# Optimization experiments

Measured on AMD Instinct MI355X. Metric: run time of the kernel, lower is better.

Reference implementation:

```python
import jax, jax.numpy as jnp
import numpy as np
from jax import lax

LATENT = 64
NUM_EMB = 512
BETA = 0.25
DN = ('NCHW', 'OIHW', 'NCHW')


def conv(x, w, b, stride, pad):
    y = lax.conv_general_dilated(x, w, (stride, stride), [(pad, pad), (pad, pad)],
                                 dimension_numbers=DN)
    return y + b[None, :, None, None]


def tconv(x, w, b, stride, pad, opad):
    # torch ConvTranspose2d(k=3, stride, padding=pad, output_padding=opad)
    # == dilated conv with lhs_dilation=stride, padding (k-1-pad, k-1-pad+opad),
    #    spatially-flipped kernel. w is stored OIHW (out, in, kh, kw).
    k = w.shape[2]
    lo, hi = k - 1 - pad, k - 1 - pad + opad
    y = lax.conv_general_dilated(x, w[:, :, ::-1, ::-1], (1, 1), [(lo, hi), (lo, hi)],
                                 lhs_dilation=(stride, stride), dimension_numbers=DN)
    return y + b[None, :, None, None]


def vector_quantize(z, codebook):
    # z: (B, D, H, W); codebook: (K, D)
    B, D, H, W = z.shape
    flat = z.transpose(0, 2, 3, 1).reshape(-1, D)  # (BHW, D)
    d = (jnp.sum(flat ** 2, axis=1, keepdims=True)
         + jnp.sum(codebook ** 2, axis=1)
         - 2.0 * flat @ codebook.T)  # (BHW, K)
    idx = jnp.argmin(d, axis=1)
    q = codebook[idx].reshape(B, H, W, D).transpose(0, 3, 1, 2)  # (B, D, H, W)
    commitment = jnp.mean((lax.stop_gradient(q) - z) ** 2)
    codebook_loss = jnp.mean((q - lax.stop_gradient(z)) ** 2)
    loss = BETA * commitment + codebook_loss
    q_ste = z + lax.stop_gradient(q - z)  # straight-through estimator
    return q_ste, loss


def setup_inputs() -> dict:
    key = jax.random.key(0)
    ks = jax.random.split(key, 16)
    f32 = jnp.float32
    inp = {
        'x': jax.random.uniform(ks[0], (1024, 1, 50, 50), dtype=f32),
        'enc_w1': jax.random.normal(ks[1], (32, 1, 3, 3), f32) * 0.1,
        'enc_b1': jnp.zeros((32,), f32),
        'enc_w2': jax.random.normal(ks[2], (64, 32, 3, 3), f32) * 0.05,
        'enc_b2': jnp.zeros((64,), f32),
        'enc_w3': jax.random.normal(ks[3], (LATENT, 64, 1, 1), f32) * 0.1,
        'enc_b3': jnp.zeros((LATENT,), f32),
        'codebook': jax.random.uniform(ks[4], (NUM_EMB, LATENT), dtype=f32),
        'dec_w1': jax.random.normal(ks[5], (64, LATENT, 3, 3), f32) * 0.05,
        'dec_b1': jnp.zeros((64,), f32),
        'dec_w2': jax.random.normal(ks[6], (32, 64, 3, 3), f32) * 0.05,
        'dec_b2': jnp.zeros((32,), f32),
        'dec_w3': jax.random.normal(ks[7], (1, 32, 3, 3), f32) * 0.05,
        'dec_b3': jnp.zeros((1,), f32),
    }
    return inp


def reference(x, enc_w1, enc_b1, enc_w2, enc_b2, enc_w3, enc_b3, codebook,
              dec_w1, dec_b1, dec_w2, dec_b2, dec_w3, dec_b3):
    # encoder: (B,1,50,50) -> (B,LATENT,13,13)
    h = jax.nn.relu(conv(x, enc_w1, enc_b1, 2, 1))
    h = jax.nn.relu(conv(h, enc_w2, enc_b2, 2, 1))
    z = conv(h, enc_w3, enc_b3, 1, 0)
    q, vq_loss = vector_quantize(z, codebook)
    # decoder: 13 -> 25 -> 50
    h = jax.nn.relu(tconv(q, dec_w1, dec_b1, 2, 1, 0))
    h = jax.nn.relu(tconv(h, dec_w2, dec_b2, 2, 1, 1))
    x_recon = jax.nn.sigmoid(conv(h, dec_w3, dec_b3, 1, 1))
    return x_recon, vq_loss
```

## Files before the change

### kernel.cpp

```cpp
#include <hip/hip_runtime.h>
#include <math.h>


typedef __attribute__((ext_vector_type(8))) short s8v;
typedef __attribute__((ext_vector_type(4))) float f4v;
typedef __attribute__((ext_vector_type(4))) int i4v;

__device__ inline unsigned short f2bf(float f) {
    unsigned u = __builtin_bit_cast(unsigned, f);
    return (unsigned short)((u + 0x7fffu + ((u >> 16) & 1u)) >> 16);
}
__device__ inline float bf2f(unsigned short h) {
    return __builtin_bit_cast(float, ((unsigned)h) << 16);
}

__global__ __launch_bounds__(256) void k_prep_all(
        const float* __restrict__ cb,  const float* __restrict__ ew2,
        const float* __restrict__ ew3, const float* __restrict__ dw1,
        const float* __restrict__ dw2,
        unsigned short* __restrict__ cbm, unsigned short* __restrict__ wB2n,
        unsigned short* __restrict__ wB1, unsigned short* __restrict__ wB2,
        unsigned short* __restrict__ wB3, float* __restrict__ cn,
        float* __restrict__ loss) {
    int i = blockIdx.x * 256 + threadIdx.x;
    if (i < 98304) {
        int j = i & 7, lane = (i >> 3) & 63;
        int kc = (i >> 9) % 6, nt = (i >> 9) / 6;
        int n = nt * 16 + (lane & 15);
        int k = kc * 32 + ((lane >> 4) << 3) + j;
        int seg = k >> 6, kk = k & 63;
        float c = cb[n * 64 + kk];
        unsigned short ch = f2bf(c);
        cbm[i] = (seg == 1) ? f2bf(c - bf2f(ch)) : ch;
    } else if (i < 153600) {
        int q = i - 98304;
        int j = q & 7, lane = (q >> 3) & 63;
        int kc = (q >> 9) % 27, nt = (q >> 9) / 27;
        int k = kc * 32 + ((lane >> 4) << 3) + j;
        int co = nt * 16 + (lane & 15);
        int part = (k < 288) ? 0 : (k < 576) ? 1 : 0;
        int kk = (k < 288) ? k : (k < 576) ? k - 288 : k - 576;
        int tap = kk >> 5, ci = kk & 31;
        float v = ew2[(co * 32 + ci) * 9 + tap];
        unsigned short hi = f2bf(v);
        wB2n[q] = part ? f2bf(v - bf2f(hi)) : hi;
    } else if (i < 219136) {
        int q = i - 153600;
        int j = q & 7, l = (q >> 3) & 63, kc = (q >> 9) & 7, nt = q >> 12;
        int n = nt * 16 + (l & 15), k = kc * 32 + (l >> 4) * 8 + j;
        int cls = n >> 6, co = n & 63, p = k >> 6, ci = k & 63;
        int jh = -1, jw = -1;
        if (cls == 0)      { if (p == 0) { jh = 1; jw = 1; } }
        else if (cls == 1) { if (p == 1) { jh = 1; jw = 0; } else if (p == 0) { jh = 1; jw = 2; } }
        else if (cls == 2) { if (p == 2) { jh = 0; jw = 1; } else if (p == 0) { jh = 2; jw = 1; } }
        else { if (p == 3) { jh = 0; jw = 0; } else if (p == 2) { jh = 0; jw = 2; }
               else if (p == 1) { jh = 2; jw = 0; } else { jh = 2; jw = 2; } }
        float v = (jh >= 0) ? dw1[((co * 64 + ci) * 3 + jh) * 3 + jw] : 0.f;
        wB1[q] = f2bf(v);
    } else if (i < 251904) {
        int q = i - 219136;
        int j = q & 7, l = (q >> 3) & 63, kc = (q >> 9) & 7, nt = q >> 12;
        int n = nt * 16 + (l & 15), k = kc * 32 + (l >> 4) * 8 + j;
        int cls = n >> 5, co = n & 31, p = k >> 6, ci = k & 63;
        int jh = -1, jw = -1;
        if (cls == 0)      { if (p == 0) { jh = 1; jw = 1; } }
        else if (cls == 1) { if (p == 1) { jh = 1; jw = 0; } else if (p == 0) { jh = 1; jw = 2; } }
        else if (cls == 2) { if (p == 2) { jh = 0; jw = 1; } else if (p == 0) { jh = 2; jw = 1; } }
        else { if (p == 3) { jh = 0; jw = 0; } else if (p == 2) { jh = 0; jw = 2; }
               else if (p == 1) { jh = 2; jw = 0; } else { jh = 2; jw = 2; } }
        float v = (jh >= 0) ? dw2[((co * 64 + ci) * 3 + jh) * 3 + jw] : 0.f;
        wB2[q] = f2bf(v);
    } else if (i < 264192) {
        int q = i - 251904;
        int j = q & 7, lane = (q >> 3) & 63;
        int kc = (q >> 9) % 6, nt = (q >> 9) / 6;
        int k = kc * 32 + ((lane >> 4) << 3) + j;
        int n = nt * 16 + (lane & 15);
        int part = (k < 64) ? 0 : (k < 128) ? 1 : 0;
        int kk = (k < 64) ? k : (k < 128) ? k - 64 : k - 128;
        float v = ew3[n * 64 + kk];
        unsigned short hi = f2bf(v);
        wB3[q] = part ? f2bf(v - bf2f(hi)) : hi;
    } else if (i < 264704) {
        int k = i - 264192;
        const float* r = cb + k * 64;
        float s = 0.f;
#pragma unroll
        for (int c = 0; c < 64; ++c) s += r[c] * r[c];
        cn[k] = s;
    } else if (i == 264704) {
        *loss = 0.f;
    }
}

__global__ __launch_bounds__(256) void k_conv1(const float* __restrict__ x,
                                               const float* __restrict__ w,
                                               const float* __restrict__ b,
                                               float* __restrict__ h1, int total) {
    __shared__ float4 wl4[72];
    float* wl = (float*)wl4;
    int tid = threadIdx.x;
    for (int t = tid; t < 288; t += 256) {
        int tap = t >> 5, co = t & 31;
        wl[t] = w[co * 9 + tap];
    }
    __syncthreads();
    int pix = blockIdx.x * 256 + tid;
    if (pix >= total) return;
    int n = pix / 625, p = pix % 625, oh = p / 25, ow = p % 25;
    const float* xp = x + (size_t)n * 2500;
    float4 a[8];
#pragma unroll
    for (int j = 0; j < 8; ++j) a[j] = ((const float4*)b)[j];
#pragma unroll
    for (int kh = 0; kh < 3; ++kh) {
        int ih = 2 * oh - 1 + kh;
        if ((unsigned)ih >= 50u) continue;
#pragma unroll
        for (int kw = 0; kw < 3; ++kw) {
            int iw = 2 * ow - 1 + kw;
            if ((unsigned)iw >= 50u) continue;
            float v = xp[ih * 50 + iw];
            int tap = kh * 3 + kw;
#pragma unroll
            for (int j = 0; j < 8; ++j) {
                float4 ww = wl4[tap * 8 + j];
                a[j].x += v * ww.x; a[j].y += v * ww.y;
                a[j].z += v * ww.z; a[j].w += v * ww.w;
            }
        }
    }
    float4* op = (float4*)(h1 + (size_t)pix * 32);
#pragma unroll
    for (int j = 0; j < 8; ++j) {
        float4 r;
        r.x = fmaxf(a[j].x, 0.f); r.y = fmaxf(a[j].y, 0.f);
        r.z = fmaxf(a[j].z, 0.f); r.w = fmaxf(a[j].w, 0.f);
        op[j] = r;
    }
}

__global__ __launch_bounds__(256) void k_enc_m(const float* __restrict__ h1,
                                               const unsigned short* __restrict__ B2n,
                                               const unsigned short* __restrict__ B3,
                                               const float* __restrict__ b2,
                                               const float* __restrict__ b3,
                                               float* __restrict__ z, int npix) {
    __shared__ short a1[16 * 872];
    __shared__ short a2[16 * 200];
    __shared__ float cz[16 * 68];
    int tid = threadIdx.x, blk = blockIdx.x;
    {
        int m = tid >> 4, chunk = tid & 15;
        if (chunk < 9) {
            int pix = blk * 16 + m;
            float4 v[8];
            const float4 zero = {0.f, 0.f, 0.f, 0.f};
            bool ok = false;
            if (pix < npix) {
                int n = pix / 169, p = pix % 169, oh = p / 13, ow = p % 13;
                int kh = chunk / 3, kw = chunk % 3;
                int ih = 2 * oh - 1 + kh, iw = 2 * ow - 1 + kw;
                ok = ((unsigned)ih < 25u) && ((unsigned)iw < 25u);
                if (ok) {
                    const float4* ip = (const float4*)(h1 + (((size_t)n * 25 + ih) * 25 + iw) * 32);
#pragma unroll
                    for (int c4 = 0; c4 < 8; ++c4) v[c4] = ip[c4];
                }
            }
            if (!ok) {
#pragma unroll
                for (int c4 = 0; c4 < 8; ++c4) v[c4] = zero;
            }
            unsigned short hi[32], lo[32];
#pragma unroll
            for (int c4 = 0; c4 < 8; ++c4) {
                float vv[4] = {v[c4].x, v[c4].y, v[c4].z, v[c4].w};
#pragma unroll
                for (int e = 0; e < 4; ++e) {
                    int ci = c4 * 4 + e;
                    unsigned short h = f2bf(vv[e]);
                    hi[ci] = h;
                    lo[ci] = f2bf(vv[e] - bf2f(h));
                }
            }
            short* row = a1 + m * 872 + chunk * 32;
            i4v* d0 = (i4v*)row;
            i4v* d1 = (i4v*)(row + 288);
            i4v* d2 = (i4v*)(row + 576);
#pragma unroll
            for (int g = 0; g < 4; ++g) {
                i4v ph, pl;
#pragma unroll
                for (int e = 0; e < 4; ++e) {
                    int b0 = g * 8 + e * 2;
                    ph[e] = (int)((unsigned)hi[b0] | ((unsigned)hi[b0 + 1] << 16));
                    pl[e] = (int)((unsigned)lo[b0] | ((unsigned)lo[b0 + 1] << 16));
                }
                d0[g] = ph; d1[g] = ph; d2[g] = pl;
            }
        }
    }
    __syncthreads();
    int wave = tid >> 6, lane = tid & 63;
    int arow1 = (lane & 15) * 872 + (lane >> 4) * 8;
    f4v acc = (f4v){0.f, 0.f, 0.f, 0.f};
#pragma unroll
    for (int kc = 0; kc < 27; ++kc) {
        s8v a = *(const s8v*)(a1 + arow1 + kc * 32);
        s8v b = *(const s8v*)((const short*)B2n + ((size_t)((wave * 27 + kc) * 64 + lane)) * 8);
        acc = __builtin_amdgcn_mfma_f32_16x16x32_bf16(a, b, acc, 0, 0, 0);
    }
    {
        float bv = b2[wave * 16 + (lane & 15)];
        int n = wave * 16 + (lane & 15);
#pragma unroll
        for (int r = 0; r < 4; ++r) {
            int m = (lane >> 4) * 4 + r;
            float h = fmaxf(acc[r] + bv, 0.f);
            unsigned short hh = f2bf(h);
            unsigned short ll = f2bf(h - bf2f(hh));
            a2[m * 200 + n] = (short)hh;
            a2[m * 200 + 64 + n] = (short)hh;
            a2[m * 200 + 128 + n] = (short)ll;
        }
    }
    __syncthreads();
    int arow2 = (lane & 15) * 200 + (lane >> 4) * 8;
    f4v acc2 = (f4v){0.f, 0.f, 0.f, 0.f};
#pragma unroll
    for (int kc = 0; kc < 6; ++kc) {
        s8v a = *(const s8v*)(a2 + arow2 + kc * 32);
        s8v b = *(const s8v*)((const short*)B3 + ((size_t)((wave * 6 + kc) * 64 + lane)) * 8);
        acc2 = __builtin_amdgcn_mfma_f32_16x16x32_bf16(a, b, acc2, 0, 0, 0);
    }
    {
        float bv = b3[wave * 16 + (lane & 15)];
        int n = wave * 16 + (lane & 15);
#pragma unroll
        for (int r = 0; r < 4; ++r) {
            int m = (lane >> 4) * 4 + r;
            cz[m * 68 + n] = acc2[r] + bv;
        }
    }
    __syncthreads();
    {
        int m = tid >> 4, c4 = tid & 15;
        int pix = blk * 16 + m;
        if (pix < npix) {
            float4 v = *(float4*)(cz + m * 68 + c4 * 4);
            *(float4*)(z + (size_t)pix * 64 + c4 * 4) = v;
        }
    }
}

__global__ __launch_bounds__(256) void k_vq_m(const float* __restrict__ z,
                                              const float* __restrict__ cb,
                                              const unsigned short* __restrict__ cbm,
                                              const float* __restrict__ cn,
                                              float* __restrict__ q,
                                              float* __restrict__ loss, int npix) {
    __shared__ short a_lds[32 * 200];
    __shared__ float reds[4 * 32];
    __shared__ int   redk[4 * 32];
    __shared__ int   bkf[32];
    __shared__ float lred[4];
    int tid = threadIdx.x, blk = blockIdx.x;
    {
        int m = tid >> 3, p = tid & 7;
        int pix = blk * 32 + m;
        unsigned short zh[8], zl[8];
        if (pix < npix) {
            const float* src = z + (size_t)pix * 64 + p * 8;
#pragma unroll
            for (int v = 0; v < 8; ++v) {
                float f = src[v];
                unsigned short h = f2bf(f);
                zh[v] = h; zl[v] = f2bf(f - bf2f(h));
            }
        } else {
#pragma unroll
            for (int v = 0; v < 8; ++v) { zh[v] = 0; zl[v] = 0; }
        }
        unsigned ph[4], pl[4];
#pragma unroll
        for (int v = 0; v < 4; ++v) {
            ph[v] = (unsigned)zh[2 * v] | ((unsigned)zh[2 * v + 1] << 16);
            pl[v] = (unsigned)zl[2 * v] | ((unsigned)zl[2 * v + 1] << 16);
        }
        short* row = a_lds + m * 200;
        i4v vh = (i4v){(int)ph[0], (int)ph[1], (int)ph[2], (int)ph[3]};
        i4v vl = (i4v){(int)pl[0], (int)pl[1], (int)pl[2], (int)pl[3]};
        *(i4v*)(row + p * 8) = vh;
        *(i4v*)(row + 64 + p * 8) = vh;
        *(i4v*)(row + 128 + p * 8) = vl;
    }
    __syncthreads();
    int wave = tid >> 6, lane = tid & 63;
    s8v af[2][6];
#pragma unroll
    for (int mt = 0; mt < 2; ++mt) {
        int arow = (mt * 16 + (lane & 15)) * 200 + (lane >> 4) * 8;
#pragma unroll
        for (int kc = 0; kc < 6; ++kc)
            af[mt][kc] = *(const s8v*)(a_lds + arow + kc * 32);
    }
    float bd[2][4];
    int bk[2][4];
#pragma unroll
    for (int mt = 0; mt < 2; ++mt)
#pragma unroll
        for (int r = 0; r < 4; ++r) { bd[mt][r] = 3.4e38f; bk[mt][r] = 0; }
#pragma unroll 2
    for (int nt = 0; nt < 8; ++nt) {
        int ntg = wave * 8 + nt;
        s8v bf[6];
#pragma unroll
        for (int kc = 0; kc < 6; ++kc)
            bf[kc] = *(const s8v*)((const short*)cbm + ((size_t)((ntg * 6 + kc) * 64 + lane)) * 8);
        f4v acc0 = (f4v){0.f, 0.f, 0.f, 0.f};
        f4v acc1 = (f4v){0.f, 0.f, 0.f, 0.f};
#pragma unroll
        for (int kc = 0; kc < 6; ++kc) {
            acc0 = __builtin_amdgcn_mfma_f32_16x16x32_bf16(af[0][kc], bf[kc], acc0, 0, 0, 0);
            acc1 = __builtin_amdgcn_mfma_f32_16x16x32_bf16(af[1][kc], bf[kc], acc1, 0, 0, 0);
        }
        int kcol = ntg * 16 + (lane & 15);
        float cnk = cn[kcol];
#pragma unroll
        for (int r = 0; r < 4; ++r) {
            float d0 = cnk - 2.f * acc0[r];
            if (d0 < bd[0][r]) { bd[0][r] = d0; bk[0][r] = kcol; }
            float d1 = cnk - 2.f * acc1[r];
            if (d1 < bd[1][r]) { bd[1][r] = d1; bk[1][r] = kcol; }
        }
    }
#pragma unroll
    for (int off = 1; off < 16; off <<= 1) {
#pragma unroll
        for (int mt = 0; mt < 2; ++mt)
#pragma unroll
            for (int r = 0; r < 4; ++r) {
                float od = __shfl_xor(bd[mt][r], off);
                int ok = __shfl_xor(bk[mt][r], off);
                if (od < bd[mt][r] || (od == bd[mt][r] && ok < bk[mt][r])) {
                    bd[mt][r] = od; bk[mt][r] = ok;
                }
            }
    }
    if ((lane & 15) == 0) {
#pragma unroll
        for (int mt = 0; mt < 2; ++mt)
#pragma unroll
            for (int r = 0; r < 4; ++r) {
                int m = mt * 16 + (lane >> 4) * 4 + r;
                reds[wave * 32 + m] = bd[mt][r];
                redk[wave * 32 + m] = bk[mt][r];
            }
    }
    __syncthreads();
    if (tid < 32) {
        float d0 = reds[tid]; int k0 = redk[tid];
#pragma unroll
        for (int w = 1; w < 4; ++w) {
            float dw = reds[w * 32 + tid]; int kw = redk[w * 32 + tid];
            if (dw < d0 || (dw == d0 && kw < k0)) { d0 = dw; k0 = kw; }
        }
        bkf[tid] = k0;
    }
    __syncthreads();
    float lsum = 0.f;
#pragma unroll
    for (int it = 0; it < 2; ++it) {
        int m = tid >> 3, c4 = (tid & 7) + it * 8;
        int pix = blk * 32 + m;
        if (pix < npix) {
            int k0 = bkf[m];
            float4 cq = ((const float4*)cb)[(size_t)k0 * 16 + c4];
            float4 zz = ((const float4*)(z + (size_t)pix * 64))[c4];
            float dx = cq.x - zz.x, dy = cq.y - zz.y, dz = cq.z - zz.z, dw = cq.w - zz.w;
            lsum += dx * dx + dy * dy + dz * dz + dw * dw;
            ((float4*)(q + (size_t)pix * 64))[c4] = cq;
        }
    }
#pragma unroll
    for (int off = 32; off > 0; off >>= 1) lsum += __shfl_down(lsum, off);
    if ((tid & 63) == 0) lred[tid >> 6] = lsum;
    __syncthreads();
    if (tid == 0) {
        float t = lred[0] + lred[1] + lred[2] + lred[3];
        atomicAdd(loss, t * (1.25f / 11075584.f));
    }
}

__global__ __launch_bounds__(256) void k_tconv1_m(const float* __restrict__ q,
                                                  const unsigned short* __restrict__ wB,
                                                  const float* __restrict__ bias,
                                                  unsigned short* __restrict__ d1,
                                                  int nquad) {
    __shared__ short a_lds[32 * 264];
    __shared__ short c_lds[32 * 264];
    int tid = threadIdx.x, blk = blockIdx.x;
#pragma unroll
    for (int pass = 0; pass < 4; ++pass) {
        int idx = tid + pass * 256;
        int m = idx >> 5, sub = idx & 31;
        int qg = blk * 32 + m;
        int p = sub >> 3, ci0 = (sub & 7) * 8;
        unsigned short t8[8];
        bool have = false;
        if (qg < nquad) {
            int img = qg / 169, r = qg % 169, qm = r / 13, qw = r % 13;
            int sm = qm + (p >> 1), sw = qw + (p & 1);
            if (sm < 13 && sw < 13) {
                const float* src = q + (((size_t)img * 13 + sm) * 13 + sw) * 64 + ci0;
#pragma unroll
                for (int v = 0; v < 8; ++v) t8[v] = f2bf(src[v]);
                have = true;
            }
        }
        if (!have) {
#pragma unroll
            for (int v = 0; v < 8; ++v) t8[v] = 0;
        }
        i4v pk;
#pragma unroll
        for (int e = 0; e < 4; ++e)
            pk[e] = (int)((unsigned)t8[2 * e] | ((unsigned)t8[2 * e + 1] << 16));
        *(i4v*)(a_lds + m * 264 + sub * 8) = pk;
    }
    __syncthreads();
    int wave = tid >> 6, lane = tid & 63;
    f4v acc[2][4];
#pragma unroll
    for (int mt = 0; mt < 2; ++mt)
#pragma unroll
        for (int i = 0; i < 4; ++i) acc[mt][i] = (f4v){0.f, 0.f, 0.f, 0.f};
    float bv[4];
#pragma unroll
    for (int i = 0; i < 4; ++i) bv[i] = bias[((wave * 4 + i) * 16 + (lane & 15)) & 63];
#pragma unroll
    for (int kc = 0; kc < 8; ++kc) {
        s8v a0 = *(const s8v*)(a_lds + ((lane & 15)) * 264 + (lane >> 4) * 8 + kc * 32);
        s8v a1 = *(const s8v*)(a_lds + (16 + (lane & 15)) * 264 + (lane >> 4) * 8 + kc * 32);
#pragma unroll
        for (int i = 0; i < 4; ++i) {
            int nt = wave * 4 + i;
            s8v b = *(const s8v*)((const short*)wB + ((size_t)((nt * 8 + kc) * 64 + lane)) * 8);
            acc[0][i] = __builtin_amdgcn_mfma_f32_16x16x32_bf16(a0, b, acc[0][i], 0, 0, 0);
            acc[1][i] = __builtin_amdgcn_mfma_f32_16x16x32_bf16(a1, b, acc[1][i], 0, 0, 0);
        }
    }
#pragma unroll
    for (int mt = 0; mt < 2; ++mt)
#pragma unroll
        for (int i = 0; i < 4; ++i) {
            int n = (wave * 4 + i) * 16 + (lane & 15);
#pragma unroll
            for (int r2 = 0; r2 < 4; ++r2) {
                int m = mt * 16 + (lane >> 4) * 4 + r2;
                float v = fmaxf(acc[mt][i][r2] + bv[i], 0.f);
                c_lds[m * 264 + n] = (short)f2bf(v);
            }
        }
    __syncthreads();
#pragma unroll
    for (int pass = 0; pass < 4; ++pass) {
        int ch = tid + pass * 256;
        int m = ch >> 5, cpart = ch & 31;
        int qg = blk * 32 + m;
        if (qg >= nquad) continue;
        int img = qg / 169, r = qg % 169, qm = r / 13, qw = r % 13;
        int cls = cpart >> 3, co8 = (cpart & 7) * 8;
        int oh = 2 * qm + (cls >> 1), ow = 2 * qw + (cls & 1);
        if (oh >= 25 || ow >= 25) continue;
        i4v val = *(i4v*)(c_lds + m * 264 + cls * 64 + co8);
        *(i4v*)(d1 + (((size_t)img * 25 + oh) * 25 + ow) * 64 + co8) = val;
    }
}

__global__ __launch_bounds__(256) void k_tconv2_m(const unsigned short* __restrict__ d1,
                                                  const unsigned short* __restrict__ wB,
                                                  const float* __restrict__ bias,
                                                  unsigned short* __restrict__ d2,
                                                  int nquad) {
    __shared__ short a_lds[32 * 264];
    __shared__ short c_lds[32 * 136];
    int tid = threadIdx.x, blk = blockIdx.x;
#pragma unroll
    for (int pass = 0; pass < 4; ++pass) {
        int idx = tid + pass * 256;
        int m = idx >> 5, sub = idx & 31;
        int qg = blk * 32 + m;
        int p = sub >> 3, ci0 = (sub & 7) * 8;
        i4v v = (i4v){0, 0, 0, 0};
        if (qg < nquad) {
            int img = qg / 625, r = qg % 625, qm = r / 25, qw = r % 25;
            int sm = qm + (p >> 1), sw = qw + (p & 1);
            if (sm < 25 && sw < 25)
                v = *(const i4v*)(d1 + (((size_t)img * 25 + sm) * 25 + sw) * 64 + ci0);
        }
        *(i4v*)(a_lds + m * 264 + sub * 8) = v;
    }
    __syncthreads();
    int wave = tid >> 6, lane = tid & 63;
    f4v acc[2][2];
#pragma unroll
    for (int mt = 0; mt < 2; ++mt)
#pragma unroll
        for (int i = 0; i < 2; ++i) acc[mt][i] = (f4v){0.f, 0.f, 0.f, 0.f};
    float bv[2];
#pragma unroll
    for (int i = 0; i < 2; ++i) bv[i] = bias[((wave * 2 + i) * 16 + (lane & 15)) & 31];
#pragma unroll
    for (int kc = 0; kc < 8; ++kc) {
        s8v a0 = *(const s8v*)(a_lds + ((lane & 15)) * 264 + (lane >> 4) * 8 + kc * 32);
        s8v a1 = *(const s8v*)(a_lds + (16 + (lane & 15)) * 264 + (lane >> 4) * 8 + kc * 32);
#pragma unroll
        for (int i = 0; i < 2; ++i) {
            int nt = wave * 2 + i;
            s8v b = *(const s8v*)((const short*)wB + ((size_t)((nt * 8 + kc) * 64 + lane)) * 8);
            acc[0][i] = __builtin_amdgcn_mfma_f32_16x16x32_bf16(a0, b, acc[0][i], 0, 0, 0);
            acc[1][i] = __builtin_amdgcn_mfma_f32_16x16x32_bf16(a1, b, acc[1][i], 0, 0, 0);
        }
    }
#pragma unroll
    for (int mt = 0; mt < 2; ++mt)
#pragma unroll
        for (int i = 0; i < 2; ++i) {
            int n = (wave * 2 + i) * 16 + (lane & 15);
#pragma unroll
            for (int r2 = 0; r2 < 4; ++r2) {
                int m = mt * 16 + (lane >> 4) * 4 + r2;
                float v = fmaxf(acc[mt][i][r2] + bv[i], 0.f);
                c_lds[m * 136 + n] = (short)f2bf(v);
            }
        }
    __syncthreads();
#pragma unroll
    for (int pass = 0; pass < 2; ++pass) {
        int ch = tid + pass * 256;
        int m = ch >> 4, cpart = ch & 15;
        int qg = blk * 32 + m;
        if (qg >= nquad) continue;
        int img = qg / 625, r = qg % 625, qm = r / 25, qw = r % 25;
        int cls = cpart >> 2, co8 = (cpart & 3) * 8;
        int oh = 2 * qm + (cls >> 1), ow = 2 * qw + (cls & 1);
        i4v val = *(i4v*)(c_lds + m * 136 + cls * 32 + co8);
        *(i4v*)(d2 + (((size_t)img * 50 + oh) * 50 + ow) * 32 + co8) = val;
    }
}

__global__ __launch_bounds__(256) void k_convf(const unsigned short* __restrict__ in,
                                               const float* __restrict__ w,
                                               const float* __restrict__ b,
                                               float* __restrict__ out, int total) {
    __shared__ float wl[288];
    int tid = threadIdx.x;
    for (int t = tid; t < 288; t += 256) {
        int tap = t >> 5, ci = t & 31;
        wl[t] = w[ci * 9 + tap];
    }
    __syncthreads();
    int pix = blockIdx.x * 256 + tid;
    if (pix >= total) return;
    int n = pix / 2500, p = pix % 2500, oh = p / 50, ow = p % 50;
    float acc = b[0];
#pragma unroll
    for (int kh = 0; kh < 3; ++kh) {
        int ih = oh - 1 + kh;
        if ((unsigned)ih >= 50u) continue;
#pragma unroll
        for (int kw = 0; kw < 3; ++kw) {
            int iw = ow - 1 + kw;
            if ((unsigned)iw >= 50u) continue;
            const float* wt = wl + (kh * 3 + kw) * 32;
            const i4v* ip4 = (const i4v*)(in + (((size_t)n * 50 + ih) * 50 + iw) * 32);
#pragma unroll
            for (int c8 = 0; c8 < 4; ++c8) {
                i4v u = ip4[c8];
#pragma unroll
                for (int e = 0; e < 4; ++e) {
                    unsigned uu = (unsigned)u[e];
                    float x0 = __builtin_bit_cast(float, uu << 16);
                    float x1 = __builtin_bit_cast(float, uu & 0xffff0000u);
                    acc = fmaf(x0, wt[c8 * 8 + e * 2], acc);
                    acc = fmaf(x1, wt[c8 * 8 + e * 2 + 1], acc);
                }
            }
        }
    }
    out[pix] = 1.f / (1.f + expf(-acc));
}

extern "C" void kernel_launch(void* const* d_in, const int* in_sizes, int n_in,
                              void* d_out, int out_size, void* d_ws, size_t ws_size,
                              hipStream_t stream) {
    const float* x   = (const float*)d_in[0];
    const float* ew1 = (const float*)d_in[1];
    const float* eb1 = (const float*)d_in[2];
    const float* ew2 = (const float*)d_in[3];
    const float* eb2 = (const float*)d_in[4];
    const float* ew3 = (const float*)d_in[5];
    const float* eb3 = (const float*)d_in[6];
    const float* cb  = (const float*)d_in[7];
    const float* dw1 = (const float*)d_in[8];
    const float* db1 = (const float*)d_in[9];
    const float* dw2 = (const float*)d_in[10];
    const float* db2 = (const float*)d_in[11];
    const float* dw3 = (const float*)d_in[12];
    const float* db3 = (const float*)d_in[13];
    float* out = (float*)d_out;
    float* loss = out + 2560000;

    float* ws = (float*)d_ws;
    float* cn = ws;
    unsigned short* wB1  = (unsigned short*)(ws + 512);
    unsigned short* wB2  = (unsigned short*)(ws + 33280);
    unsigned short* wB2n = (unsigned short*)(ws + 49664);
    unsigned short* wB3  = (unsigned short*)(ws + 77312);
    unsigned short* cbm  = (unsigned short*)(ws + 83456);
    const size_t tw_floats = 132608;

    const int B = 1024;
    const size_t A_per = 40000, B_per = 20000;
    size_t avail = (ws_size / 4 > tw_floats) ? ws_size / 4 - tw_floats : 0;
    int BC = (int)(avail / (A_per + B_per));
    if (BC > B) BC = B;
    if (BC < 1) BC = 1;
    float* regA = ws + tw_floats;
    float* regB = regA + (size_t)BC * A_per;

    k_prep_all<<<1035, 256, 0, stream>>>(cb, ew2, ew3, dw1, dw2,
                                         cbm, wB2n, wB1, wB2, wB3, cn, loss);

    for (int n0 = 0; n0 < B; n0 += BC) {
        int bc = (B - n0 < BC) ? (B - n0) : BC;
        const float* xch = x + (size_t)n0 * 2500;

        int t1 = bc * 625;
        k_conv1<<<(t1 + 255) / 256, 256, 0, stream>>>(xch, ew1, eb1, regA, t1);

        int npix = bc * 169;
        k_enc_m<<<(npix + 15) / 16, 256, 0, stream>>>(regA, wB2n, wB3, eb2, eb3, regB, npix);

        k_vq_m<<<(npix + 31) / 32, 256, 0, stream>>>(regB, cb, cbm, cn, regA, loss, npix);

        unsigned short* d1 = (unsigned short*)regB;
        k_tconv1_m<<<(npix + 31) / 32, 256, 0, stream>>>(regA, wB1, db1, d1, npix);

        int nq2 = bc * 625;
        unsigned short* d2 = (unsigned short*)regA;
        k_tconv2_m<<<(nq2 + 31) / 32, 256, 0, stream>>>(d1, wB2, db2, d2, nq2);

        int t6 = bc * 2500;
        k_convf<<<(t6 + 255) / 256, 256, 0, stream>>>(d2, dw3, db3, out + (size_t)n0 * 2500, t6);
    }
}
```

Before: 505.0 us.

## Store intermediates as pre-split bf16 hi/lo pairs instead of fp32

The conv1 output and the encoder latent are now written as bf16 hi/lo split pairs rather than fp32. Consumers can then copy them straight into LDS without re-splitting, and the split is no longer repeated for every 3x3 tap read in k_enc_m. The quantized output q is stored as single bf16, halving its traffic, and the VQ loss reconstructs z from the hi/lo copy already in LDS. Byte counts stay the same for h1 and z, so the gain comes mainly from removed conversion ALU work and the smaller q.

Measured after the change: 495.5 us. About the same (-1.9%).

```diff
diff --git a/kernel.cpp b/kernel.cpp
--- a/kernel.cpp
+++ b/kernel.cpp
@@ -5,6 +5,7 @@
 typedef __attribute__((ext_vector_type(8))) short s8v;
 typedef __attribute__((ext_vector_type(4))) float f4v;
 typedef __attribute__((ext_vector_type(4))) int i4v;
+typedef __attribute__((ext_vector_type(4))) short s4v;
 
 __device__ inline unsigned short f2bf(float f) {
     unsigned u = __builtin_bit_cast(unsigned, f);
@@ -96,7 +97,8 @@
 __global__ __launch_bounds__(256) void k_conv1(const float* __restrict__ x,
                                                const float* __restrict__ w,
                                                const float* __restrict__ b,
-                                               float* __restrict__ h1, int total) {
+                                               unsigned short* __restrict__ h1,
+                                               int total) {
     __shared__ float4 wl4[72];
     float* wl = (float*)wl4;
     int tid = threadIdx.x;
@@ -130,58 +132,61 @@
             }
         }
     }
-    float4* op = (float4*)(h1 + (size_t)pix * 32);
+    unsigned short hi[32], lo[32];
 #pragma unroll
     for (int j = 0; j < 8; ++j) {
-        float4 r;
-        r.x = fmaxf(a[j].x, 0.f); r.y = fmaxf(a[j].y, 0.f);
-        r.z = fmaxf(a[j].z, 0.f); r.w = fmaxf(a[j].w, 0.f);
-        op[j] = r;
-    }
-}
-
-__global__ __launch_bounds__(256) void k_enc_m(const float* __restrict__ h1,
+        float vv[4] = {a[j].x, a[j].y, a[j].z, a[j].w};
+#pragma unroll
+        for (int e = 0; e < 4; ++e) {
+            float v = fmaxf(vv[e], 0.f);
+            unsigned short h = f2bf(v);
+            hi[j * 4 + e] = h;
+            lo[j * 4 + e] = f2bf(v - bf2f(h));
+        }
+    }
+    i4v* op = (i4v*)(h1 + (size_t)pix * 64);
+#pragma unroll
+    for (int g = 0; g < 4; ++g) {
+        i4v ph, pl;
+#pragma unroll
+        for (int e = 0; e < 4; ++e) {
+            int b0 = g * 8 + e * 2;
+            ph[e] = (int)((unsigned)hi[b0] | ((unsigned)hi[b0 + 1] << 16));
+            pl[e] = (int)((unsigned)lo[b0] | ((unsigned)lo[b0 + 1] << 16));
+        }
+        op[g] = ph;
+        op[4 + g] = pl;
+    }
+}
+
+__global__ __launch_bounds__(256) void k_enc_m(const unsigned short* __restrict__ h1,
                                                const unsigned short* __restrict__ B2n,
                                                const unsigned short* __restrict__ B3,
                                                const float* __restrict__ b2,
                                                const float* __restrict__ b3,
-                                               float* __restrict__ z, int npix) {
+                                               unsigned short* __restrict__ z, int npix) {
     __shared__ short a1[16 * 872];
     __shared__ short a2[16 * 200];
-    __shared__ float cz[16 * 68];
+    __shared__ short czs[16 * 136];
     int tid = threadIdx.x, blk = blockIdx.x;
     {
         int m = tid >> 4, chunk = tid & 15;
         if (chunk < 9) {
             int pix = blk * 16 + m;
-            float4 v[8];
-            const float4 zero = {0.f, 0.f, 0.f, 0.f};
-            bool ok = false;
+            i4v vh[4], vl[4];
+#pragma unroll
+            for (int g = 0; g < 4; ++g) {
+                vh[g] = (i4v){0, 0, 0, 0};
+                vl[g] = (i4v){0, 0, 0, 0};
+            }
             if (pix < npix) {
                 int n = pix / 169, p = pix % 169, oh = p / 13, ow = p % 13;
                 int kh = chunk / 3, kw = chunk % 3;
                 int ih = 2 * oh - 1 + kh, iw = 2 * ow - 1 + kw;
-                ok = ((unsigned)ih < 25u) && ((unsigned)iw < 25u);
-                if (ok) {
-                    const float4* ip = (const float4*)(h1 + (((size_t)n * 25 + ih) * 25 + iw) * 32);
-#pragma unroll
-                    for (int c4 = 0; c4 < 8; ++c4) v[c4] = ip[c4];
-                }
-            }
-            if (!ok) {
-#pragma unroll
-                for (int c4 = 0; c4 < 8; ++c4) v[c4] = zero;
-            }
-            unsigned short hi[32], lo[32];
-#pragma unroll
-            for (int c4 = 0; c4 < 8; ++c4) {
-                float vv[4] = {v[c4].x, v[c4].y, v[c4].z, v[c4].w};
-#pragma unroll
-                for (int e = 0; e < 4; ++e) {
-                    int ci = c4 * 4 + e;
-                    unsigned short h = f2bf(vv[e]);
-                    hi[ci] = h;
-                    lo[ci] = f2bf(vv[e] - bf2f(h));
+                if (((unsigned)ih < 25u) && ((unsigned)iw < 25u)) {
+                    const i4v* ip = (const i4v*)(h1 + (((size_t)n * 25 + ih) * 25 + iw) * 64);
+#pragma unroll
+                    for (int g = 0; g < 4; ++g) { vh[g] = ip[g]; vl[g] = ip[4 + g]; }
                 }
             }
             short* row = a1 + m * 872 + chunk * 32;
@@ -189,16 +194,7 @@
             i4v* d1 = (i4v*)(row + 288);
             i4v* d2 = (i4v*)(row + 576);
 #pragma unroll
-            for (int g = 0; g < 4; ++g) {
-                i4v ph, pl;
-#pragma unroll
-                for (int e = 0; e < 4; ++e) {
-                    int b0 = g * 8 + e * 2;
-                    ph[e] = (int)((unsigned)hi[b0] | ((unsigned)hi[b0 + 1] << 16));
-                    pl[e] = (int)((unsigned)lo[b0] | ((unsigned)lo[b0 + 1] << 16));
-                }
-                d0[g] = ph; d1[g] = ph; d2[g] = pl;
-            }
+            for (int g = 0; g < 4; ++g) { d0[g] = vh[g]; d1[g] = vh[g]; d2[g] = vl[g]; }
         }
     }
     __syncthreads();
@@ -240,25 +236,26 @@
 #pragma unroll
         for (int r = 0; r < 4; ++r) {
             int m = (lane >> 4) * 4 + r;
-            cz[m * 68 + n] = acc2[r] + bv;
+            float v = acc2[r] + bv;
+            unsigned short hh = f2bf(v);
+            czs[m * 136 + n] = (short)hh;
+            czs[m * 136 + 64 + n] = (short)f2bf(v - bf2f(hh));
         }
     }
     __syncthreads();
     {
-        int m = tid >> 4, c4 = tid & 15;
+        int m = tid >> 4, t = tid & 15;
         int pix = blk * 16 + m;
-        if (pix < npix) {
-            float4 v = *(float4*)(cz + m * 68 + c4 * 4);
-            *(float4*)(z + (size_t)pix * 64 + c4 * 4) = v;
-        }
-    }
-}
-
-__global__ __launch_bounds__(256) void k_vq_m(const float* __restrict__ z,
+        if (pix < npix)
+            *(i4v*)(z + (size_t)pix * 128 + t * 8) = *(i4v*)(czs + m * 136 + t * 8);
+    }
+}
+
+__global__ __launch_bounds__(256) void k_vq_m(const unsigned short* __restrict__ z,
                                               const float* __restrict__ cb,
                                               const unsigned short* __restrict__ cbm,
                                               const float* __restrict__ cn,
-                                              float* __restrict__ q,
+                                              unsigned short* __restrict__ q,
                                               float* __restrict__ loss, int npix) {
     __shared__ short a_lds[32 * 200];
     __shared__ float reds[4 * 32];
@@ -269,28 +266,14 @@
     {
         int m = tid >> 3, p = tid & 7;
         int pix = blk * 32 + m;
-        unsigned short zh[8], zl[8];
+        i4v vh = (i4v){0, 0, 0, 0};
+        i4v vl = (i4v){0, 0, 0, 0};
         if (pix < npix) {
-            const float* src = z + (size_t)pix * 64 + p * 8;
-#pragma unroll
-            for (int v = 0; v < 8; ++v) {
-                float f = src[v];
-                unsigned short h = f2bf(f);
-                zh[v] = h; zl[v] = f2bf(f - bf2f(h));
-            }
-        } else {
-#pragma unroll
-            for (int v = 0; v < 8; ++v) { zh[v] = 0; zl[v] = 0; }
-        }
-        unsigned ph[4], pl[4];
-#pragma unroll
-        for (int v = 0; v < 4; ++v) {
-            ph[v] = (unsigned)zh[2 * v] | ((unsigned)zh[2 * v + 1] << 16);
-            pl[v] = (unsigned)zl[2 * v] | ((unsigned)zl[2 * v + 1] << 16);
+            const i4v* src = (const i4v*)(z + (size_t)pix * 128);
+            vh = src[p];
+            vl = src[8 + p];
         }
         short* row = a_lds + m * 200;
-        i4v vh = (i4v){(int)ph[0], (int)ph[1], (int)ph[2], (int)ph[3]};
-        i4v vl = (i4v){(int)pl[0], (int)pl[1], (int)pl[2], (int)pl[3]};
         *(i4v*)(row + p * 8) = vh;
         *(i4v*)(row + 64 + p * 8) = vh;
         *(i4v*)(row + 128 + p * 8) = vl;
@@ -377,10 +360,19 @@
         if (pix < npix) {
             int k0 = bkf[m];
             float4 cq = ((const float4*)cb)[(size_t)k0 * 16 + c4];
-            float4 zz = ((const float4*)(z + (size_t)pix * 64))[c4];
-            float dx = cq.x - zz.x, dy = cq.y - zz.y, dz = cq.z - zz.z, dw = cq.w - zz.w;
+            const short* rz = a_lds + m * 200 + c4 * 4;
+            s4v zh4 = *(const s4v*)rz;
+            s4v zl4 = *(const s4v*)(rz + 128);
+            float zx = bf2f((unsigned short)zh4[0]) + bf2f((unsigned short)zl4[0]);
+            float zy = bf2f((unsigned short)zh4[1]) + bf2f((unsigned short)zl4[1]);
+            float zz = bf2f((unsigned short)zh4[2]) + bf2f((unsigned short)zl4[2]);
+            float zw = bf2f((unsigned short)zh4[3]) + bf2f((unsigned short)zl4[3]);
+            float dx = cq.x - zx, dy = cq.y - zy, dz = cq.z - zz, dw = cq.w - zw;
             lsum += dx * dx + dy * dy + dz * dz + dw * dw;
-            ((float4*)(q + (size_t)pix * 64))[c4] = cq;
+            s4v qs;
+            qs[0] = (short)f2bf(cq.x); qs[1] = (short)f2bf(cq.y);
+            qs[2] = (short)f2bf(cq.z); qs[3] = (short)f2bf(cq.w);
+            *(s4v*)(q + (size_t)pix * 64 + c4 * 4) = qs;
         }
     }
 #pragma unroll
@@ -393,7 +385,7 @@
     }
 }
 
-__global__ __launch_bounds__(256) void k_tconv1_m(const float* __restrict__ q,
+__global__ __launch_bounds__(256) void k_tconv1_m(const unsigned short* __restrict__ q,
                                                   const unsigned short* __restrict__ wB,
                                                   const float* __restrict__ bias,
                                                   unsigned short* __restrict__ d1,
@@ -407,27 +399,14 @@
         int m = idx >> 5, sub = idx & 31;
         int qg = blk * 32 + m;
         int p = sub >> 3, ci0 = (sub & 7) * 8;
-        unsigned short t8[8];
-        bool have = false;
+        i4v v = (i4v){0, 0, 0, 0};
         if (qg < nquad) {
             int img = qg / 169, r = qg % 169, qm = r / 13, qw = r % 13;
             int sm = qm + (p >> 1), sw = qw + (p & 1);
-            if (sm < 13 && sw < 13) {
-                const float* src = q + (((size_t)img * 13 + sm) * 13 + sw) * 64 + ci0;
-#pragma unroll
-                for (int v = 0; v < 8; ++v) t8[v] = f2bf(src[v]);
-                have = true;
-            }
-        }
-        if (!have) {
-#pragma unroll
-            for (int v = 0; v < 8; ++v) t8[v] = 0;
-        }
-        i4v pk;
-#pragma unroll
-        for (int e = 0; e < 4; ++e)
-            pk[e] = (int)((unsigned)t8[2 * e] | ((unsigned)t8[2 * e + 1] << 16));
-        *(i4v*)(a_lds + m * 264 + sub * 8) = pk;
+            if (sm < 13 && sw < 13)
+                v = *(const i4v*)(q + (((size_t)img * 13 + sm) * 13 + sw) * 64 + ci0);
+        }
+        *(i4v*)(a_lds + m * 264 + sub * 8) = v;
     }
     __syncthreads();
     int wave = tid >> 6, lane = tid & 63;
@@ -639,15 +618,18 @@
         const float* xch = x + (size_t)n0 * 2500;
 
         int t1 = bc * 625;
-        k_conv1<<<(t1 + 255) / 256, 256, 0, stream>>>(xch, ew1, eb1, regA, t1);
+        unsigned short* h1p = (unsigned short*)regA;
+        k_conv1<<<(t1 + 255) / 256, 256, 0, stream>>>(xch, ew1, eb1, h1p, t1);
 
         int npix = bc * 169;
-        k_enc_m<<<(npix + 15) / 16, 256, 0, stream>>>(regA, wB2n, wB3, eb2, eb3, regB, npix);
-
-        k_vq_m<<<(npix + 31) / 32, 256, 0, stream>>>(regB, cb, cbm, cn, regA, loss, npix);
+        unsigned short* zp = (unsigned short*)regB;
+        k_enc_m<<<(npix + 15) / 16, 256, 0, stream>>>(h1p, wB2n, wB3, eb2, eb3, zp, npix);
+
+        unsigned short* qb = (unsigned short*)regA;
+        k_vq_m<<<(npix + 31) / 32, 256, 0, stream>>>(zp, cb, cbm, cn, qb, loss, npix);
 
         unsigned short* d1 = (unsigned short*)regB;
-        k_tconv1_m<<<(npix + 31) / 32, 256, 0, stream>>>(regA, wB1, db1, d1, npix);
+        k_tconv1_m<<<(npix + 31) / 32, 256, 0, stream>>>(qb, wB1, db1, d1, npix);
 
         int nq2 = bc * 625;
         unsigned short* d2 = (unsigned short*)regA;
```
